# Kernel optimization log

Hardware: AMD Instinct MI355X
Metric: run time of the kernel (lower is better)

## Reference

```python
import jax, jax.numpy as jnp
import numpy as np
from jax.scipy.special import gammaln

N_I = 100000
N_J = 100000
D = 8
S_I = 6000
S_J = 6000
NNZ = 500000
EPS = 1e-06


def setup_inputs() -> dict:
    key = jax.random.key(0)
    ks = jax.random.split(key, 9)
    beta = jax.random.normal(ks[0], (N_I,), dtype=jnp.float32)
    gamma = jax.random.normal(ks[1], (N_J,), dtype=jnp.float32)
    latent_zi = jax.random.normal(ks[2], (N_I, D), dtype=jnp.float32)
    latent_zj = jax.random.normal(ks[3], (N_J, D), dtype=jnp.float32)
    # multinomial-without-replacement node samples -> random permutation prefix
    sample_i_idx = jax.random.permutation(ks[4], N_I)[:S_I]
    sample_j_idx = jax.random.permutation(ks[5], N_J)[:S_J]
    # spspmm-selected subgraph links (global node indices) with edge counts
    sparse_i_sample = jax.random.randint(ks[6], (NNZ,), 0, N_I)
    sparse_j_sample = jax.random.randint(ks[7], (NNZ,), 0, N_J)
    valueC = jax.random.uniform(ks[8], (NNZ,), dtype=jnp.float32)
    return {
        'beta': beta, 'gamma': gamma,
        'latent_zi': latent_zi, 'latent_zj': latent_zj,
        'valueC': valueC,
        'sample_i_idx': sample_i_idx, 'sample_j_idx': sample_j_idx,
        'sparse_i_sample': sparse_i_sample, 'sparse_j_sample': sparse_j_sample,
    }


def reference(beta, gamma, latent_zi, latent_zj, valueC,
              sample_i_idx, sample_j_idx, sparse_i_sample, sparse_j_sample):
    # Dense non-link term over sampled (I, J) block
    zi = latent_zi[sample_i_idx]            # [S_I, D]
    zj = latent_zj[sample_j_idx]            # [S_J, D]
    diff = zi[:, None, :] - zj[None, :, :] + EPS   # [S_I, S_J, D]
    z_dist = jnp.sqrt(jnp.sum(diff * diff, axis=-1))  # [S_I, S_J]
    Lambda = beta[sample_i_idx][:, None] + gamma[sample_j_idx][None, :] - z_dist
    # Sparse link terms (Poisson log-likelihood)
    dl = latent_zi[sparse_i_sample] - latent_zj[sparse_j_sample] + EPS  # [NNZ, D]
    z_dist_links = jnp.sqrt(jnp.sum(dl * dl, axis=-1))                  # [NNZ]
    bias_links = beta[sparse_i_sample] + gamma[sparse_j_sample]
    log_Lambda_links = valueC * (bias_links - z_dist_links)
    LL = jnp.sum(log_Lambda_links - gammaln(valueC + 1.0)) - jnp.sum(jnp.exp(Lambda))
    return LL
```

## Files before the change

kernel.cpp:

```cpp
#include <hip/hip_runtime.h>
#include <hip/hip_fp16.h>
#include <math.h>

#define NI_TOT 100000
#define NJ_TOT 100000
#define DD 8
#define SI_N 6000
#define SJ_N 6000
#define NNZ_N 500000
#define EPSF 1e-6f
#define LOG2E 1.44269504088896f
#define INV_LOG2E 0.693147180559945f

#define TI 64
#define JPT 2
#define JTILE (256 * JPT)
#define ND_I ((SI_N + TI - 1) / TI)
#define NJT ((SJ_N + JTILE - 1) / JTILE)
#define N_DENSE_BLOCKS (ND_I * NJT)
#define LPT 2
#define SPARSE_SPAN (256 * LPT)
#define N_SPARSE_BLOCKS ((NNZ_N + SPARSE_SPAN - 1) / SPARSE_SPAN)
#define N_TOTAL_BLOCKS (N_DENSE_BLOCKS + N_SPARSE_BLOCKS)

#define NROWS (NI_TOT + NJ_TOT)
#define HZ_BYTES ((size_t)NROWS * DD * 2)
#define HB_BYTES ((size_t)NROWS * 2)
#define PARTIALS_OFF (HZ_BYTES + HB_BYTES)

#define GA1 (-0.577191652f)
#define GA2 ( 0.988205891f)
#define GA3 (-0.897056937f)
#define GA4 ( 0.918206857f)
#define GA5 (-0.756704078f)
#define GA6 ( 0.482199394f)
#define GA7 (-0.193527818f)
#define GA8 ( 0.035868343f)

__global__ __launch_bounds__(256) void pack_kernel(
    const float* __restrict__ beta, const float* __restrict__ gamma,
    const float* __restrict__ zi_all, const float* __restrict__ zj_all,
    __half* __restrict__ hz, __half* __restrict__ hb)
{
    const int r = blockIdx.x * 256 + threadIdx.x;
    if (r < NROWS) {
        const float* src = (r < NI_TOT) ? zi_all + (size_t)r * DD
                                        : zj_all + (size_t)(r - NI_TOT) * DD;
        float4 a = ((const float4*)src)[0];
        float4 b = ((const float4*)src)[1];
        __half2 h0 = __floats2half2_rn(a.x, a.y);
        __half2 h1 = __floats2half2_rn(a.z, a.w);
        __half2 h2 = __floats2half2_rn(b.x, b.y);
        __half2 h3 = __floats2half2_rn(b.z, b.w);
        uint4 u;
        u.x = *(unsigned*)&h0; u.y = *(unsigned*)&h1;
        u.z = *(unsigned*)&h2; u.w = *(unsigned*)&h3;
        ((uint4*)hz)[r] = u;
    } else if (r < 2 * NROWS) {
        const int q = r - NROWS;
        float v = (q < NI_TOT) ? beta[q] : gamma[q - NI_TOT];
        hb[q] = __float2half(v);
    }
}

__device__ __forceinline__ void unpack_row(uint4 u, float f[DD]) {
    float2 p;
    p = __half22float2(*(__half2*)&u.x); f[0] = p.x; f[1] = p.y;
    p = __half22float2(*(__half2*)&u.y); f[2] = p.x; f[3] = p.y;
    p = __half22float2(*(__half2*)&u.z); f[4] = p.x; f[5] = p.y;
    p = __half22float2(*(__half2*)&u.w); f[6] = p.x; f[7] = p.y;
}

__global__ __launch_bounds__(256) void fused_kernel(
    const float* __restrict__ beta, const float* __restrict__ gamma,
    const float* __restrict__ zi_all, const float* __restrict__ zj_all,
    const float* __restrict__ valueC,
    const int* __restrict__ si, const int* __restrict__ sj,
    const int* __restrict__ spi, const int* __restrict__ spj,
    const __half* __restrict__ hz, const __half* __restrict__ hb,
    float* __restrict__ partials, float* __restrict__ out, int mode)
{
    __shared__ float sRed[4];
    __shared__ __align__(16) float  sZi[TI * DD];
    __shared__ __align__(8)  float2 sIB[TI];

    const int t = threadIdx.x;
    float blocksum = 0.0f;

    if (blockIdx.x < N_DENSE_BLOCKS) {
        const int it = blockIdx.x % ND_I;
        const int js = blockIdx.x / ND_I;
        const int i0 = it * TI;

        for (int idx = t; idx < TI * DD; idx += 256) {
            int r = idx >> 3, d = idx & 7;
            int gi = i0 + r;
            float v = (gi < SI_N) ? zi_all[(size_t)si[gi] * DD + d] : 0.0f;
            sZi[idx] = (v + EPSF) * (-2.0f * LOG2E);
        }
        __syncthreads();
        if (t < TI) {
            int gi = i0 + t;
            float s = 0.0f;
#pragma unroll
            for (int d = 0; d < DD; ++d) {
                float m = sZi[t * DD + d];
                s = fmaf(m, m, s);
            }
            float eb = 0.0f;
            if (gi < SI_N) eb = __builtin_amdgcn_exp2f(beta[si[gi]] * LOG2E);
            sIB[t] = make_float2(0.25f * s, eb);
        }

        const int jb = js * JTILE + t * JPT;
        float zc[JPT][DD], s2[JPT], gf[JPT];
#pragma unroll
        for (int u = 0; u < JPT; ++u) {
            int gj = jb + u;
            if (gj < SJ_N) {
                int row = sj[gj];
                const float4* q = (const float4*)(zj_all + (size_t)row * DD);
                float4 q0 = q[0], q1 = q[1];
                zc[u][0]=q0.x*LOG2E; zc[u][1]=q0.y*LOG2E; zc[u][2]=q0.z*LOG2E; zc[u][3]=q0.w*LOG2E;
                zc[u][4]=q1.x*LOG2E; zc[u][5]=q1.y*LOG2E; zc[u][6]=q1.z*LOG2E; zc[u][7]=q1.w*LOG2E;
                gf[u] = __builtin_amdgcn_exp2f(gamma[row] * LOG2E);
            } else {
#pragma unroll
                for (int d = 0; d < DD; ++d) zc[u][d] = 0.0f;
                gf[u] = 0.0f;
            }
            float s = 0.0f;
#pragma unroll
            for (int d = 0; d < DD; ++d) s = fmaf(zc[u][d], zc[u][d], s);
            s2[u] = s;
        }
        __syncthreads();

        float acc[JPT] = {0.0f, 0.0f};
        float4 cr0 = *(const float4*)&sZi[0];
        float4 cr1 = *(const float4*)&sZi[4];
        float2 cib = sIB[0];
#pragma unroll 4
        for (int a = 0; a < TI; ++a) {
            float4 nr0, nr1; float2 nib;
            if (a + 1 < TI) {
                nr0 = *(const float4*)&sZi[(a + 1) * DD];
                nr1 = *(const float4*)&sZi[(a + 1) * DD + 4];
                nib = sIB[a + 1];
            }
#pragma unroll
            for (int u = 0; u < JPT; ++u) {
                float dd;
                dd = fmaf(cr0.x, zc[u][0], cib.x);
                dd = fmaf(cr0.y, zc[u][1], dd);
                dd = fmaf(cr0.z, zc[u][2], dd);
                dd = fmaf(cr0.w, zc[u][3], dd);
                dd = fmaf(cr1.x, zc[u][4], dd);
                dd = fmaf(cr1.y, zc[u][5], dd);
                dd = fmaf(cr1.z, zc[u][6], dd);
                dd = fmaf(cr1.w, zc[u][7], dd);
                float ss = fmaxf(dd + s2[u], 1e-20f);
                float dist = __builtin_amdgcn_sqrtf(ss);
                float e = __builtin_amdgcn_exp2f(-dist);
                acc[u] = fmaf(cib.y, e, acc[u]);
            }
            cr0 = nr0; cr1 = nr1; cib = nib;
        }
        float bs = 0.0f;
#pragma unroll
        for (int u = 0; u < JPT; ++u) bs = fmaf(gf[u], acc[u], bs);
        blocksum = -bs;
    } else {
        const int base = (blockIdx.x - N_DENSE_BLOCKS) * SPARSE_SPAN + t;
        float val = 0.0f;
        const uint4* hzv = (const uint4*)hz;
#pragma unroll
        for (int u = 0; u < LPT; ++u) {
            const int idx = base + u * 256;
            if (idx >= NNZ_N) continue;
            const int i = spi[idx], j = spj[idx];
            const float c = valueC[idx];
            float dist, bg;
            if (mode == 0) {
                uint4 ui = hzv[i];
                uint4 uj = hzv[NI_TOT + j];
                float fi[DD], fj[DD];
                unpack_row(ui, fi);
                unpack_row(uj, fj);
                float ss = 0.0f;
#pragma unroll
                for (int d = 0; d < DD; ++d) {
                    float df = fi[d] - fj[d] + EPSF;
                    ss = fmaf(df, df, ss);
                }
                ss = fmaxf(ss, 1e-20f);
                dist = __builtin_amdgcn_sqrtf(ss);
                bg = __half2float(hb[i]) + __half2float(hb[NI_TOT + j]);
            } else {
                const float4* zi4 = (const float4*)(zi_all + (size_t)i * DD);
                const float4* zj4 = (const float4*)(zj_all + (size_t)j * DD);
                float4 a0 = zi4[0], a1 = zi4[1];
                float4 b0 = zj4[0], b1 = zj4[1];
                float ss = 0.0f, df;
                df = a0.x-b0.x+EPSF; ss = fmaf(df,df,ss);
                df = a0.y-b0.y+EPSF; ss = fmaf(df,df,ss);
                df = a0.z-b0.z+EPSF; ss = fmaf(df,df,ss);
                df = a0.w-b0.w+EPSF; ss = fmaf(df,df,ss);
                df = a1.x-b1.x+EPSF; ss = fmaf(df,df,ss);
                df = a1.y-b1.y+EPSF; ss = fmaf(df,df,ss);
                df = a1.z-b1.z+EPSF; ss = fmaf(df,df,ss);
                df = a1.w-b1.w+EPSF; ss = fmaf(df,df,ss);
                ss = fmaxf(ss, 1e-20f);
                dist = __builtin_amdgcn_sqrtf(ss);
                bg = beta[i] + gamma[j];
            }
            float g = 1.0f + c*(GA1 + c*(GA2 + c*(GA3 + c*(GA4 + c*(GA5
                          + c*(GA6 + c*(GA7 + c*GA8)))))));
            val += c * (bg - dist) - __builtin_amdgcn_logf(g) * INV_LOG2E;
        }
        blocksum = val;
    }

    float acc = blocksum;
#pragma unroll
    for (int off = 32; off; off >>= 1) acc += __shfl_down(acc, off, 64);
    const int lane = t & 63, w = t >> 6;
    if (lane == 0) sRed[w] = acc;
    __syncthreads();
    if (t == 0) {
        float s = sRed[0] + sRed[1] + sRed[2] + sRed[3];
        if (mode) atomicAdd(out, s);
        else partials[blockIdx.x] = s;
    }
}

__global__ __launch_bounds__(256) void final_reduce_kernel(
    const float* __restrict__ p, int n, float* __restrict__ out)
{
    __shared__ float sRed[4];
    float s0 = 0.0f, s1 = 0.0f, s2 = 0.0f, s3 = 0.0f;
    int i = threadIdx.x;
    for (; i + 768 < n; i += 1024) {
        s0 += p[i]; s1 += p[i + 256]; s2 += p[i + 512]; s3 += p[i + 768];
    }
    for (; i < n; i += 256) s0 += p[i];
    float s = (s0 + s1) + (s2 + s3);
#pragma unroll
    for (int off = 32; off; off >>= 1) s += __shfl_down(s, off, 64);
    const int lane = threadIdx.x & 63, w = threadIdx.x >> 6;
    if (lane == 0) sRed[w] = s;
    __syncthreads();
    if (threadIdx.x == 0) out[0] = sRed[0] + sRed[1] + sRed[2] + sRed[3];
}

extern "C" void kernel_launch(void* const* d_in, const int* in_sizes, int n_in,
                              void* d_out, int out_size, void* d_ws, size_t ws_size,
                              hipStream_t stream) {
    const float* beta   = (const float*)d_in[0];
    const float* gamma  = (const float*)d_in[1];
    const float* zi     = (const float*)d_in[2];
    const float* zj     = (const float*)d_in[3];
    const float* valueC = (const float*)d_in[4];
    const int* si   = (const int*)d_in[5];
    const int* sjx  = (const int*)d_in[6];
    const int* spi  = (const int*)d_in[7];
    const int* spj  = (const int*)d_in[8];
    float* out = (float*)d_out;

    const int ntot = N_TOTAL_BLOCKS;
    const size_t need = PARTIALS_OFF + (size_t)ntot * sizeof(float);

    if (d_ws && ws_size >= need) {
        __half* hz = (__half*)d_ws;
        __half* hb = (__half*)((char*)d_ws + HZ_BYTES);
        float* p = (float*)((char*)d_ws + PARTIALS_OFF);
        const int packb = (2 * NROWS + 255) / 256;
        pack_kernel<<<packb, 256, 0, stream>>>(beta, gamma, zi, zj, hz, hb);
        fused_kernel<<<ntot, 256, 0, stream>>>(
            beta, gamma, zi, zj, valueC, si, sjx, spi, spj, hz, hb, p, out, 0);
        final_reduce_kernel<<<1, 256, 0, stream>>>(p, ntot, out);
    } else {
        hipMemsetAsync(out, 0, sizeof(float), stream);
        fused_kernel<<<ntot, 256, 0, stream>>>(
            beta, gamma, zi, zj, valueC, si, sjx, spi, spj,
            (const __half*)zi, (const __half*)zi, nullptr, out, 1);
    }
}
```

Before: 106.0 us.

## Use packed fp16 dot2 for dense distance inner loop and template mode

Reworks the dense pairwise-distance loop to keep zi/zj rows as packed half2 and compute the cross term with four fdot2 instructions instead of eight fp32 FMAs. Precomputes each row's squared norm in fp32 during a single staging pass into one shared array, which drops a __syncthreads. Templates the kernel on mode so the runtime branch is compiled out. Rounding the latents and scaled zi (about -4x) to fp16 lowers the precision of the distance before exp, which affects accuracy.

```diff
diff --git a/kernel.cpp b/kernel.cpp
--- a/kernel.cpp
+++ b/kernel.cpp
@@ -11,6 +11,7 @@
 #define EPSF 1e-6f
 #define LOG2E 1.44269504088896f
 #define INV_LOG2E 0.693147180559945f
+#define L2SQ (LOG2E * LOG2E)
 
 #define TI 64
 #define JPT 2
@@ -36,6 +37,30 @@
 #define GA6 ( 0.482199394f)
 #define GA7 (-0.193527818f)
 #define GA8 ( 0.035868343f)
+
+typedef _Float16 h2 __attribute__((ext_vector_type(2)));
+
+#if defined(__has_builtin)
+#if __has_builtin(__builtin_amdgcn_fdot2)
+#define HAVE_FDOT2 1
+#endif
+#endif
+
+__device__ __forceinline__ h2 u2h(unsigned u) {
+    union { unsigned v; h2 h; } c; c.v = u; return c.h;
+}
+__device__ __forceinline__ unsigned pack2h(float x, float y) {
+    union { unsigned v; h2 h; } c;
+    c.h[0] = (_Float16)x; c.h[1] = (_Float16)y;
+    return c.v;
+}
+__device__ __forceinline__ float fdot2f(h2 a, h2 b, float c) {
+#ifdef HAVE_FDOT2
+    return __builtin_amdgcn_fdot2(a, b, c, false);
+#else
+    return fmaf((float)a[0], (float)b[0], fmaf((float)a[1], (float)b[1], c));
+#endif
+}
 
 __global__ __launch_bounds__(256) void pack_kernel(
     const float* __restrict__ beta, const float* __restrict__ gamma,
@@ -50,11 +75,11 @@
         float4 b = ((const float4*)src)[1];
         __half2 h0 = __floats2half2_rn(a.x, a.y);
         __half2 h1 = __floats2half2_rn(a.z, a.w);
-        __half2 h2 = __floats2half2_rn(b.x, b.y);
+        __half2 h2v = __floats2half2_rn(b.x, b.y);
         __half2 h3 = __floats2half2_rn(b.z, b.w);
         uint4 u;
         u.x = *(unsigned*)&h0; u.y = *(unsigned*)&h1;
-        u.z = *(unsigned*)&h2; u.w = *(unsigned*)&h3;
+        u.z = *(unsigned*)&h2v; u.w = *(unsigned*)&h3;
         ((uint4*)hz)[r] = u;
     } else if (r < 2 * NROWS) {
         const int q = r - NROWS;
@@ -71,6 +96,7 @@
     p = __half22float2(*(__half2*)&u.w); f[6] = p.x; f[7] = p.y;
 }
 
+template<int MODE>
 __global__ __launch_bounds__(256) void fused_kernel(
     const float* __restrict__ beta, const float* __restrict__ gamma,
     const float* __restrict__ zi_all, const float* __restrict__ zj_all,
@@ -78,11 +104,10 @@
     const int* __restrict__ si, const int* __restrict__ sj,
     const int* __restrict__ spi, const int* __restrict__ spj,
     const __half* __restrict__ hz, const __half* __restrict__ hb,
-    float* __restrict__ partials, float* __restrict__ out, int mode)
+    float* __restrict__ partials, float* __restrict__ out)
 {
     __shared__ float sRed[4];
-    __shared__ __align__(16) float  sZi[TI * DD];
-    __shared__ __align__(8)  float2 sIB[TI];
+    __shared__ __align__(16) unsigned sRow[TI * 8];
 
     const int t = threadIdx.x;
     float blocksum = 0.0f;
@@ -92,79 +117,92 @@
         const int js = blockIdx.x / ND_I;
         const int i0 = it * TI;
 
-        for (int idx = t; idx < TI * DD; idx += 256) {
-            int r = idx >> 3, d = idx & 7;
-            int gi = i0 + r;
-            float v = (gi < SI_N) ? zi_all[(size_t)si[gi] * DD + d] : 0.0f;
-            sZi[idx] = (v + EPSF) * (-2.0f * LOG2E);
+        if (t < TI) {
+            const int gi = i0 + t;
+            uint4 mh = make_uint4(0u, 0u, 0u, 0u);
+            float seedL = 0.f, eb = 0.f;
+            if (gi < SI_N) {
+                const int row = si[gi];
+                float a[DD];
+                if (MODE == 0) {
+                    uint4 raw = ((const uint4*)hz)[row];
+                    float f[DD]; unpack_row(raw, f);
+#pragma unroll
+                    for (int d = 0; d < DD; ++d) a[d] = f[d] + EPSF;
+                } else {
+                    const float4* zp = (const float4*)(zi_all + (size_t)row * DD);
+                    float4 p0 = zp[0], p1 = zp[1];
+                    a[0]=p0.x+EPSF; a[1]=p0.y+EPSF; a[2]=p0.z+EPSF; a[3]=p0.w+EPSF;
+                    a[4]=p1.x+EPSF; a[5]=p1.y+EPSF; a[6]=p1.z+EPSF; a[7]=p1.w+EPSF;
+                }
+                float s = 0.f;
+#pragma unroll
+                for (int d = 0; d < DD; ++d) s = fmaf(a[d], a[d], s);
+                seedL = s * L2SQ;
+                eb = __builtin_amdgcn_exp2f(beta[row] * LOG2E);
+                const float k = -2.0f * L2SQ;
+                mh.x = pack2h(a[0]*k, a[1]*k);
+                mh.y = pack2h(a[2]*k, a[3]*k);
+                mh.z = pack2h(a[4]*k, a[5]*k);
+                mh.w = pack2h(a[6]*k, a[7]*k);
+            }
+            *(uint4*)&sRow[t * 8] = mh;
+            sRow[t * 8 + 4] = __float_as_uint(seedL);
+            sRow[t * 8 + 5] = __float_as_uint(eb);
         }
-        __syncthreads();
-        if (t < TI) {
-            int gi = i0 + t;
-            float s = 0.0f;
-#pragma unroll
-            for (int d = 0; d < DD; ++d) {
-                float m = sZi[t * DD + d];
-                s = fmaf(m, m, s);
-            }
-            float eb = 0.0f;
-            if (gi < SI_N) eb = __builtin_amdgcn_exp2f(beta[si[gi]] * LOG2E);
-            sIB[t] = make_float2(0.25f * s, eb);
-        }
 
         const int jb = js * JTILE + t * JPT;
-        float zc[JPT][DD], s2[JPT], gf[JPT];
+        uint4 ch[JPT]; float s2[JPT], gf[JPT];
 #pragma unroll
         for (int u = 0; u < JPT; ++u) {
             int gj = jb + u;
             if (gj < SJ_N) {
                 int row = sj[gj];
-                const float4* q = (const float4*)(zj_all + (size_t)row * DD);
-                float4 q0 = q[0], q1 = q[1];
-                zc[u][0]=q0.x*LOG2E; zc[u][1]=q0.y*LOG2E; zc[u][2]=q0.z*LOG2E; zc[u][3]=q0.w*LOG2E;
-                zc[u][4]=q1.x*LOG2E; zc[u][5]=q1.y*LOG2E; zc[u][6]=q1.z*LOG2E; zc[u][7]=q1.w*LOG2E;
+                if (MODE == 0) {
+                    ch[u] = ((const uint4*)hz)[NI_TOT + row];
+                } else {
+                    const float4* q = (const float4*)(zj_all + (size_t)row * DD);
+                    float4 q0 = q[0], q1 = q[1];
+                    ch[u].x = pack2h(q0.x, q0.y); ch[u].y = pack2h(q0.z, q0.w);
+                    ch[u].z = pack2h(q1.x, q1.y); ch[u].w = pack2h(q1.z, q1.w);
+                }
+                float s = fdot2f(u2h(ch[u].x), u2h(ch[u].x),
+                          fdot2f(u2h(ch[u].y), u2h(ch[u].y),
+                          fdot2f(u2h(ch[u].z), u2h(ch[u].z),
+                          fdot2f(u2h(ch[u].w), u2h(ch[u].w), 0.0f))));
+                s2[u] = s * L2SQ;
                 gf[u] = __builtin_amdgcn_exp2f(gamma[row] * LOG2E);
             } else {
-#pragma unroll
-                for (int d = 0; d < DD; ++d) zc[u][d] = 0.0f;
+                ch[u] = make_uint4(0u, 0u, 0u, 0u);
+                s2[u] = 0.0f;
                 gf[u] = 0.0f;
             }
-            float s = 0.0f;
-#pragma unroll
-            for (int d = 0; d < DD; ++d) s = fmaf(zc[u][d], zc[u][d], s);
-            s2[u] = s;
         }
         __syncthreads();
 
         float acc[JPT] = {0.0f, 0.0f};
-        float4 cr0 = *(const float4*)&sZi[0];
-        float4 cr1 = *(const float4*)&sZi[4];
-        float2 cib = sIB[0];
+        uint4  cr  = *(const uint4*)&sRow[0];
+        float2 cib = *(const float2*)&sRow[4];
 #pragma unroll 4
         for (int a = 0; a < TI; ++a) {
-            float4 nr0, nr1; float2 nib;
+            uint4 nr; float2 nib;
             if (a + 1 < TI) {
-                nr0 = *(const float4*)&sZi[(a + 1) * DD];
-                nr1 = *(const float4*)&sZi[(a + 1) * DD + 4];
-                nib = sIB[a + 1];
+                nr  = *(const uint4*)&sRow[(a + 1) * 8];
+                nib = *(const float2*)&sRow[(a + 1) * 8 + 4];
             }
 #pragma unroll
             for (int u = 0; u < JPT; ++u) {
                 float dd;
-                dd = fmaf(cr0.x, zc[u][0], cib.x);
-                dd = fmaf(cr0.y, zc[u][1], dd);
-                dd = fmaf(cr0.z, zc[u][2], dd);
-                dd = fmaf(cr0.w, zc[u][3], dd);
-                dd = fmaf(cr1.x, zc[u][4], dd);
-                dd = fmaf(cr1.y, zc[u][5], dd);
-                dd = fmaf(cr1.z, zc[u][6], dd);
-                dd = fmaf(cr1.w, zc[u][7], dd);
+                dd = fdot2f(u2h(cr.x), u2h(ch[u].x), cib.x);
+                dd = fdot2f(u2h(cr.y), u2h(ch[u].y), dd);
+                dd = fdot2f(u2h(cr.z), u2h(ch[u].z), dd);
+                dd = fdot2f(u2h(cr.w), u2h(ch[u].w), dd);
                 float ss = fmaxf(dd + s2[u], 1e-20f);
                 float dist = __builtin_amdgcn_sqrtf(ss);
                 float e = __builtin_amdgcn_exp2f(-dist);
                 acc[u] = fmaf(cib.y, e, acc[u]);
             }
-            cr0 = nr0; cr1 = nr1; cib = nib;
+            cr = nr; cib = nib;
         }
         float bs = 0.0f;
 #pragma unroll
@@ -181,7 +219,7 @@
             const int i = spi[idx], j = spj[idx];
             const float c = valueC[idx];
             float dist, bg;
-            if (mode == 0) {
+            if (MODE == 0) {
                 uint4 ui = hzv[i];
                 uint4 uj = hzv[NI_TOT + j];
                 float fi[DD], fj[DD];
@@ -229,7 +267,7 @@
     __syncthreads();
     if (t == 0) {
         float s = sRed[0] + sRed[1] + sRed[2] + sRed[3];
-        if (mode) atomicAdd(out, s);
+        if (MODE) atomicAdd(out, s);
         else partials[blockIdx.x] = s;
     }
 }
@@ -276,13 +314,13 @@
         float* p = (float*)((char*)d_ws + PARTIALS_OFF);
         const int packb = (2 * NROWS + 255) / 256;
         pack_kernel<<<packb, 256, 0, stream>>>(beta, gamma, zi, zj, hz, hb);
-        fused_kernel<<<ntot, 256, 0, stream>>>(
-            beta, gamma, zi, zj, valueC, si, sjx, spi, spj, hz, hb, p, out, 0);
+        fused_kernel<0><<<ntot, 256, 0, stream>>>(
+            beta, gamma, zi, zj, valueC, si, sjx, spi, spj, hz, hb, p, out);
         final_reduce_kernel<<<1, 256, 0, stream>>>(p, ntot, out);
     } else {
         hipMemsetAsync(out, 0, sizeof(float), stream);
-        fused_kernel<<<ntot, 256, 0, stream>>>(
+        fused_kernel<1><<<ntot, 256, 0, stream>>>(
             beta, gamma, zi, zj, valueC, si, sjx, spi, spj,
-            (const __half*)zi, (const __half*)zi, nullptr, out, 1);
-    }
-}
+            (const __half*)zi, (const __half*)zi, nullptr, out);
+    }
+}
```

After: 106.7 us. About the same (+0.7%).
